# Kernel optimization log

Hardware: AMD Instinct MI355X
Metric: run time of the kernel (lower is better)

Reference implementation:

```python
import jax, jax.numpy as jnp
import numpy as np


def setup_inputs() -> dict:
    key = jax.random.key(0)
    ks = jax.random.split(key, 8)
    B, C, H, W = 8, 256, 64, 64
    inter = max(1, C // 8)  # inter_dim = in_dim // 8
    sc = 1.0 / np.sqrt(C)   # ~ conv kaiming-uniform scale
    return {
        "x": jax.random.normal(ks[0], (B, C, H, W), jnp.float32),
        "Wq": jax.random.normal(ks[1], (inter, C), jnp.float32) * sc,
        "bq": jax.random.normal(ks[2], (inter,), jnp.float32) * sc,
        "Wk": jax.random.normal(ks[3], (inter, C), jnp.float32) * sc,
        "bk": jax.random.normal(ks[4], (inter,), jnp.float32) * sc,
        "Wv": jax.random.normal(ks[5], (C, C), jnp.float32) * sc,
        "bv": jax.random.normal(ks[6], (C,), jnp.float32) * sc,
        # gamma is nn.Parameter(torch.zeros(1)); use small nonzero so the
        # attention branch actually contributes to the output.
        "gamma": jax.random.normal(ks[7], (1,), jnp.float32) * 0.1,
    }


def reference(x, Wq, bq, Wk, bk, Wv, bv, gamma):
    B, C, H, W = x.shape
    N = H * W
    xf = x.reshape(B, C, N)                                  # flatten spatial
    # 1x1 convs == per-pixel linear projections
    q = jnp.einsum('ic,bcn->bin', Wq, xf) + bq[None, :, None]  # [B, inter, N]
    k = jnp.einsum('ic,bcn->bin', Wk, xf) + bk[None, :, None]  # [B, inter, N]
    v = jnp.einsum('oc,bcn->bon', Wv, xf) + bv[None, :, None]  # [B, C, N]
    # energy[b,n,m] = sum_i q[b,i,n] * k[b,i,m]  (unscaled, non-causal)
    energy = jnp.einsum('bin,bim->bnm', q, k)                # [B, N, N]
    attention = jax.nn.softmax(energy, axis=-1)
    # attn_output[b,c,m] = sum_n attention[b,m,n] * v[b,c,n]
    attn_output = jnp.einsum('bmn,bcn->bcm', attention, v).reshape(B, C, H, W)
    return gamma[0] * attn_output + x
```

## Files before the change

### kernel.cpp

```cpp
#include <hip/hip_runtime.h>
#include <hip/hip_bf16.h>

#define BB 8
#define CC 256
#define NN 4096
#define II 32

typedef __bf16 bf16_t;
typedef bf16_t bf16x8 __attribute__((ext_vector_type(8)));
typedef float f32x4 __attribute__((ext_vector_type(4)));

__global__ __launch_bounds__(256) void wconv(
    const float* __restrict__ Wq, const float* __restrict__ Wk,
    const float* __restrict__ Wv, bf16_t* __restrict__ Wb) {
  int idx = blockIdx.x * 256 + threadIdx.x;
  int o = idx >> 8, c = idx & 255;
  float w = (o < 32) ? Wq[o * 256 + c]
          : (o < 64) ? Wk[(o - 32) * 256 + c]
                     : Wv[(o - 64) * 256 + c];
  Wb[idx] = (bf16_t)w;
}

__global__ __launch_bounds__(256, 2) void qkv_fused(
    const float* __restrict__ x, const bf16_t* __restrict__ Wb,
    const float* __restrict__ bq, const float* __restrict__ bk,
    const float* __restrict__ bv,
    bf16_t* __restrict__ q, bf16_t* __restrict__ k, bf16_t* __restrict__ v) {
  __shared__ bf16_t xs[128][264];

  const int t  = threadIdx.x;
  const int n0 = blockIdx.x * 128;
  const int og = blockIdx.y;
  const int b  = blockIdx.z;

  {
    const float* xb = x + (size_t)b * CC * NN + n0;
    const int cq  = t >> 2;
    const int nq4 = (t & 3) * 4;
#pragma unroll
    for (int p = 0; p < 8; ++p) {
      const int nb = p * 16 + nq4;
      float4 r0 = *(const float4*)&xb[(size_t)(cq * 4 + 0) * NN + nb];
      float4 r1 = *(const float4*)&xb[(size_t)(cq * 4 + 1) * NN + nb];
      float4 r2 = *(const float4*)&xb[(size_t)(cq * 4 + 2) * NN + nb];
      float4 r3 = *(const float4*)&xb[(size_t)(cq * 4 + 3) * NN + nb];
      float c0[4] = {r0.x, r0.y, r0.z, r0.w};
      float c1[4] = {r1.x, r1.y, r1.z, r1.w};
      float c2[4] = {r2.x, r2.y, r2.z, r2.w};
      float c3[4] = {r3.x, r3.y, r3.z, r3.w};
#pragma unroll
      for (int jj = 0; jj < 4; ++jj) {
        union { bf16_t h[4]; uint2 u; } pk;
        pk.h[0] = (bf16_t)c0[jj]; pk.h[1] = (bf16_t)c1[jj];
        pk.h[2] = (bf16_t)c2[jj]; pk.h[3] = (bf16_t)c3[jj];
        *(uint2*)&xs[nb + jj][cq * 4] = pk.u;
      }
    }
  }
  __syncthreads();

  const int w  = t >> 6;
  const int l  = t & 63;
  const int lo = l & 15;
  const int q4 = l >> 4;
  const int nbase = n0 + w * 32;

  f32x4 acc[10][2];
#pragma unroll
  for (int ot = 0; ot < 10; ++ot)
#pragma unroll
    for (int ms = 0; ms < 2; ++ms) acc[ot][ms] = (f32x4){0.f, 0.f, 0.f, 0.f};

#pragma unroll 2
  for (int ks = 0; ks < 8; ++ks) {
    const int c0 = ks * 32 + q4 * 8;
    bf16x8 af[2];
#pragma unroll
    for (int ms = 0; ms < 2; ++ms)
      af[ms] = *(const bf16x8*)&xs[w * 32 + ms * 16 + lo][c0];
    bf16x8 bw[10];
#pragma unroll
    for (int ot = 0; ot < 10; ++ot)
      bw[ot] = *(const bf16x8*)&Wb[((og * 10 + ot) * 16 + lo) * 256 + c0];
#pragma unroll
    for (int ms = 0; ms < 2; ++ms)
#pragma unroll
      for (int ot = 0; ot < 10; ++ot)
        acc[ot][ms] = __builtin_amdgcn_mfma_f32_16x16x32_bf16(
            af[ms], bw[ot], acc[ot][ms], 0, 0, 0);
  }

#pragma unroll
  for (int ot = 0; ot < 10; ++ot) {
    const int gt = og * 10 + ot;
    if (gt < 4) {
      const bool isq = gt < 2;
      const int i = (gt & 1) * 16 + lo;
      const float bias = isq ? bq[i] : bk[i];
      bf16_t* dst = (isq ? q : k) + (size_t)b * NN * II;
#pragma unroll
      for (int ms = 0; ms < 2; ++ms) {
#pragma unroll
        for (int r = 0; r < 4; ++r) {
          int n = nbase + ms * 16 + q4 * 4 + r;
          dst[(size_t)n * II + i] = (bf16_t)(acc[ot][ms][r] + bias);
        }
      }
    } else {
      const int ctg = gt - 4;
      const float bias = bv[ctg * 16 + lo];
      bf16_t* dst = v + (size_t)b * CC * NN;
#pragma unroll
      for (int ms = 0; ms < 2; ++ms) {
        union { bf16_t h[4]; uint2 u; } pk;
#pragma unroll
        for (int r = 0; r < 4; ++r) pk.h[r] = (bf16_t)(acc[ot][ms][r] + bias);
        const size_t idx =
            (((size_t)ctg * 512 + (nbase >> 3) + ms * 2 + (q4 >> 1)) * 16 + lo) * 8
            + (q4 & 1) * 4;
        *(uint2*)&dst[idx] = pk.u;
      }
    }
  }
}

__global__ __launch_bounds__(256, 2) void attn_mfma(
    const bf16_t* __restrict__ q, const bf16_t* __restrict__ k,
    const bf16_t* __restrict__ v, const float* __restrict__ x,
    const float* __restrict__ gamma, float* __restrict__ out) {
  __shared__ bf16_t Pld[2][64 * 64];
  __shared__ float lred[16][64];
  __shared__ float lfin[64];

  const int t  = threadIdx.x;
  const int w  = t >> 6;
  const int l  = t & 63;
  const int lo = l & 15;
  const int q4 = l >> 4;
  const int bid = blockIdx.x;
  const int b   = bid & 7;
  const int m0  = (bid >> 3) * 64;

  const bf16_t* qb = q + (size_t)b * NN * II;
  const bf16_t* kb = k + (size_t)b * NN * II;
  const bf16_t* vb = v + (size_t)b * CC * NN;

  bf16x8 qf[4];
#pragma unroll
  for (int mt = 0; mt < 4; ++mt)
    qf[mt] = *(const bf16x8*)(qb + (size_t)(m0 + mt * 16 + lo) * II + q4 * 8);

  f32x4 acc[4][4];
#pragma unroll
  for (int ct = 0; ct < 4; ++ct)
#pragma unroll
    for (int mt = 0; mt < 4; ++mt) acc[ct][mt] = (f32x4){0.f, 0.f, 0.f, 0.f};
  float lp[4] = {0.f, 0.f, 0.f, 0.f};

  const f32x4 zero = (f32x4){0.f, 0.f, 0.f, 0.f};

  bf16x8 kf = *(const bf16x8*)(kb + (size_t)(w * 16 + lo) * II + q4 * 8);

  for (int n1 = 0, it = 0; n1 < NN; n1 += 64, ++it) {
    bf16x8 vf[8];
#pragma unroll
    for (int kc = 0; kc < 2; ++kc)
#pragma unroll
      for (int ct = 0; ct < 4; ++ct)
        vf[kc * 4 + ct] = *(const bf16x8*)(vb +
            ((size_t)(w * 4 + ct) * 512 + (n1 >> 3) + kc * 4) * 128 + l * 8);
    const int n_next = (n1 + 64) & (NN - 1);
    bf16x8 kf_next = *(const bf16x8*)(kb + (size_t)(n_next + w * 16 + lo) * II + q4 * 8);

    bf16_t* Pb = Pld[it & 1];
#pragma unroll
    for (int mt = 0; mt < 4; ++mt) {
      f32x4 s = __builtin_amdgcn_mfma_f32_16x16x32_bf16(kf, qf[mt], zero, 0, 0, 0);
      float e0 = __expf(s[0]), e1 = __expf(s[1]), e2 = __expf(s[2]), e3 = __expf(s[3]);
      lp[mt] += (e0 + e1) + (e2 + e3);
      union { bf16_t h[4]; uint2 u2; } ph;
      ph.h[0] = (bf16_t)e0; ph.h[1] = (bf16_t)e1;
      ph.h[2] = (bf16_t)e2; ph.h[3] = (bf16_t)e3;
      int m_loc = mt * 16 + lo;
      int c8    = w * 2 + (q4 >> 1);
      int elem  = m_loc * 64 + ((c8 ^ (m_loc & 7)) * 8) + (q4 & 1) * 4;
      *(uint2*)&Pb[elem] = ph.u2;
    }

    asm volatile("s_waitcnt lgkmcnt(0)" ::: "memory");
    __builtin_amdgcn_s_barrier();
    __builtin_amdgcn_sched_barrier(0);

#pragma unroll
    for (int kc = 0; kc < 2; ++kc) {
      bf16x8 pf[4];
#pragma unroll
      for (int mt = 0; mt < 4; ++mt) {
        int m_loc = mt * 16 + lo;
        int c8    = kc * 4 + q4;
        pf[mt] = *(const bf16x8*)&Pb[m_loc * 64 + ((c8 ^ (m_loc & 7)) * 8)];
      }
      __builtin_amdgcn_s_setprio(1);
#pragma unroll
      for (int ct = 0; ct < 4; ++ct)
#pragma unroll
        for (int mt = 0; mt < 4; ++mt)
          acc[ct][mt] = __builtin_amdgcn_mfma_f32_16x16x32_bf16(
              vf[kc * 4 + ct], pf[mt], acc[ct][mt], 0, 0, 0);
      __builtin_amdgcn_s_setprio(0);
    }
    kf = kf_next;
  }

#pragma unroll
  for (int mt = 0; mt < 4; ++mt) lred[w * 4 + q4][mt * 16 + lo] = lp[mt];
  __syncthreads();
  if (t < 64) {
    float s = 0.f;
#pragma unroll
    for (int j = 0; j < 16; ++j) s += lred[j][t];
    lfin[t] = s;
  }
  __syncthreads();

  const float g = gamma[0];
  float linv[4];
#pragma unroll
  for (int mt = 0; mt < 4; ++mt) linv[mt] = 1.0f / lfin[mt * 16 + lo];

  const int cbase = w * 64;
#pragma unroll
  for (int ct = 0; ct < 4; ++ct) {
#pragma unroll
    for (int r = 0; r < 4; ++r) {
      int c = cbase + ct * 16 + q4 * 4 + r;
      const float* xrow = x + ((size_t)b * CC + c) * NN + m0;
      float* orow       = out + ((size_t)b * CC + c) * NN + m0;
#pragma unroll
      for (int mt = 0; mt < 4; ++mt) {
        int m = mt * 16 + lo;
        orow[m] = g * acc[ct][mt][r] * linv[mt] + xrow[m];
      }
    }
  }
}

extern "C" void kernel_launch(void* const* d_in, const int* in_sizes, int n_in,
                              void* d_out, int out_size, void* d_ws, size_t ws_size,
                              hipStream_t stream) {
  const float* x     = (const float*)d_in[0];
  const float* Wq    = (const float*)d_in[1];
  const float* bq    = (const float*)d_in[2];
  const float* Wk    = (const float*)d_in[3];
  const float* bk    = (const float*)d_in[4];
  const float* Wv    = (const float*)d_in[5];
  const float* bv    = (const float*)d_in[6];
  const float* gamma = (const float*)d_in[7];
  float* out = (float*)d_out;

  bf16_t* ws = (bf16_t*)d_ws;
  bf16_t* q  = ws;
  bf16_t* k  = q + (size_t)BB * NN * II;
  bf16_t* v  = k + (size_t)BB * NN * II;
  bf16_t* Wb = v + (size_t)BB * CC * NN;

  wconv<<<dim3(320), 256, 0, stream>>>(Wq, Wk, Wv, Wb);

  dim3 gp(NN / 128, 2, BB);
  qkv_fused<<<gp, 256, 0, stream>>>(x, Wb, bq, bk, bv, q, k, v);

  attn_mfma<<<dim3(512), 256, 0, stream>>>(q, k, v, x, gamma, out);
}
```

Baseline: 195.1 us.

## Stage V tiles through LDS via async global_load_lds and use exp2 softmax

Replaces per-iteration register loads of V in the attention loop with asynchronous global-to-LDS copies issued after the PV MFMAs for the next tile. This frees VGPRs and lets the V fetch overlap with the QK/exp phase. Separately, it folds log2(e) into Wq and bq so the softmax can use the hardware exp2 instruction directly instead of __expf. The change adds a per-wave LDS buffer and a vmcnt wait before the barrier. It also adds a risk that the single-buffered V staging serializes if the loads are not complete by the time the next iteration needs them.

```diff
diff --git a/kernel.cpp b/kernel.cpp
--- a/kernel.cpp
+++ b/kernel.cpp
@@ -5,6 +5,16 @@
 #define CC 256
 #define NN 4096
 #define II 32
+#define LOG2E 1.4426950408889634f
+
+#if __has_builtin(__builtin_amdgcn_exp2f)
+#define EXP2F(x) __builtin_amdgcn_exp2f(x)
+#else
+#define EXP2F(x) exp2f(x)
+#endif
+
+#define AS1 __attribute__((address_space(1)))
+#define AS3 __attribute__((address_space(3)))
 
 typedef __bf16 bf16_t;
 typedef bf16_t bf16x8 __attribute__((ext_vector_type(8)));
@@ -15,7 +25,7 @@
     const float* __restrict__ Wv, bf16_t* __restrict__ Wb) {
   int idx = blockIdx.x * 256 + threadIdx.x;
   int o = idx >> 8, c = idx & 255;
-  float w = (o < 32) ? Wq[o * 256 + c]
+  float w = (o < 32) ? Wq[o * 256 + c] * LOG2E
           : (o < 64) ? Wk[(o - 32) * 256 + c]
                      : Wv[(o - 64) * 256 + c];
   Wb[idx] = (bf16_t)w;
@@ -96,7 +106,7 @@
     if (gt < 4) {
       const bool isq = gt < 2;
       const int i = (gt & 1) * 16 + lo;
-      const float bias = isq ? bq[i] : bk[i];
+      const float bias = isq ? bq[i] * LOG2E : bk[i];
       bf16_t* dst = (isq ? q : k) + (size_t)b * NN * II;
 #pragma unroll
       for (int ms = 0; ms < 2; ++ms) {
@@ -129,6 +139,7 @@
     const bf16_t* __restrict__ v, const float* __restrict__ x,
     const float* __restrict__ gamma, float* __restrict__ out) {
   __shared__ bf16_t Pld[2][64 * 64];
+  __shared__ bf16_t Vld[4][8][512];
   __shared__ float lred[16][64];
   __shared__ float lfin[64];
 
@@ -159,16 +170,23 @@
 
   const f32x4 zero = (f32x4){0.f, 0.f, 0.f, 0.f};
 
+#define STAGE_V(NT)                                                           \
+  {                                                                           \
+    _Pragma("unroll")                                                         \
+    for (int kc = 0; kc < 2; ++kc)                                            \
+      _Pragma("unroll")                                                       \
+      for (int ct = 0; ct < 4; ++ct) {                                        \
+        const bf16_t* gp = vb +                                               \
+            ((size_t)(w * 4 + ct) * 512 + ((NT) >> 3) + kc * 4) * 128 + l * 8;\
+        __builtin_amdgcn_global_load_lds((const AS1 void*)gp,                 \
+            (AS3 void*)&Vld[w][kc * 4 + ct][0], 16, 0, 0);                    \
+      }                                                                       \
+  }
+
+  STAGE_V(0)
   bf16x8 kf = *(const bf16x8*)(kb + (size_t)(w * 16 + lo) * II + q4 * 8);
 
   for (int n1 = 0, it = 0; n1 < NN; n1 += 64, ++it) {
-    bf16x8 vf[8];
-#pragma unroll
-    for (int kc = 0; kc < 2; ++kc)
-#pragma unroll
-      for (int ct = 0; ct < 4; ++ct)
-        vf[kc * 4 + ct] = *(const bf16x8*)(vb +
-            ((size_t)(w * 4 + ct) * 512 + (n1 >> 3) + kc * 4) * 128 + l * 8);
     const int n_next = (n1 + 64) & (NN - 1);
     bf16x8 kf_next = *(const bf16x8*)(kb + (size_t)(n_next + w * 16 + lo) * II + q4 * 8);
 
@@ -176,7 +194,8 @@
 #pragma unroll
     for (int mt = 0; mt < 4; ++mt) {
       f32x4 s = __builtin_amdgcn_mfma_f32_16x16x32_bf16(kf, qf[mt], zero, 0, 0, 0);
-      float e0 = __expf(s[0]), e1 = __expf(s[1]), e2 = __expf(s[2]), e3 = __expf(s[3]);
+      float e0 = EXP2F(s[0]), e1 = EXP2F(s[1]);
+      float e2 = EXP2F(s[2]), e3 = EXP2F(s[3]);
       lp[mt] += (e0 + e1) + (e2 + e3);
       union { bf16_t h[4]; uint2 u2; } ph;
       ph.h[0] = (bf16_t)e0; ph.h[1] = (bf16_t)e1;
@@ -187,7 +206,7 @@
       *(uint2*)&Pb[elem] = ph.u2;
     }
 
-    asm volatile("s_waitcnt lgkmcnt(0)" ::: "memory");
+    asm volatile("s_waitcnt vmcnt(0) lgkmcnt(0)" ::: "memory");
     __builtin_amdgcn_s_barrier();
     __builtin_amdgcn_sched_barrier(0);
 
@@ -202,13 +221,19 @@
       }
       __builtin_amdgcn_s_setprio(1);
 #pragma unroll
-      for (int ct = 0; ct < 4; ++ct)
+      for (int ct = 0; ct < 4; ++ct) {
+        const bf16x8 vfc = *(const bf16x8*)&Vld[w][kc * 4 + ct][l * 8];
 #pragma unroll
         for (int mt = 0; mt < 4; ++mt)
           acc[ct][mt] = __builtin_amdgcn_mfma_f32_16x16x32_bf16(
-              vf[kc * 4 + ct], pf[mt], acc[ct][mt], 0, 0, 0);
+              vfc, pf[mt], acc[ct][mt], 0, 0, 0);
+      }
       __builtin_amdgcn_s_setprio(0);
     }
+
+    __builtin_amdgcn_sched_barrier(0);
+    asm volatile("s_waitcnt lgkmcnt(0)" ::: "memory");
+    STAGE_V(n_next)
     kf = kf_next;
   }
 
```

Measured after the change: 208.6 us. +6.9%, slower.
